# Optimization experiments

Hardware: AMD Instinct MI355X
Metric: run time of the kernel (lower is better)

The kernel has to match this reference:

```python
import jax, jax.numpy as jnp
import numpy as np

N, D1, D2, B = 8, 2048, 1024, 512
D = D1 * D2
MAXBW = 3
NUM_PART = 5          # num_possible_partitions
TEMP = 0.01           # TEMPERATURE used in df_lt
DENOS = (3.0, 5.0, 17.0)  # 2^2-1, 2^2+1, 2^4+1


def ste_floor(x):
    # straight-through floor: forward floor, backward identity
    return x + jax.lax.stop_gradient(jnp.floor(x) - x)


def segmented_mean(piece, scheme, msp):
    """Replicates the inner python scan over sorted rows.
    piece:  (N, D) sorted residual errors
    scheme: (N-1, D) rounded split decisions (0/1), per column
    msp:    (N-1, D) soft split probabilities (grad factors), per column
    Returns (N, D): each row gets grad_ * (segment mean) of its segment.
    """
    n = piece.shape[0]
    buf = jnp.zeros_like(piece[0])
    cnt = jnp.zeros_like(piece[0])
    g = jnp.ones_like(piece[0])
    reset = jnp.zeros(piece.shape[1], dtype=bool)
    vlist, blist = [], []
    for i in range(n):
        buf = jnp.where(reset, piece[i], buf + piece[i])
        cnt = jnp.where(reset, 1.0, cnt + 1.0)
        g = jnp.where(reset, 1.0, g)
        if i == n - 1:
            vlist.append(g * (buf / cnt))
            blist.append(jnp.ones_like(reset))
        else:
            b = scheme[i] > 0.5
            vlist.append(jnp.where(b, g * msp[i], 0.0) * (buf / cnt))
            blist.append(b)
            g = jnp.where(b, g, g * (1.0 - msp[i]))
            reset = b
    # broadcast each segment-end value back to all rows of its segment
    out = vlist[-1]
    outs = [out]
    for i in range(n - 2, -1, -1):
        out = jnp.where(blist[i], vlist[i], out)
        outs.append(out)
    return jnp.stack(outs[::-1], axis=0)


def residual_quant(U, vsum, s, thr):
    """One residual quantization level (the update_partition=True branch)."""
    res = U - vsum                                   # (N, D)
    idx_maps = jnp.argsort(res, axis=0)              # torch.sort ascending, dim=0
    sorted_err = jnp.take_along_axis(res, idx_maps, axis=0)
    delta = sorted_err[1:] - sorted_err[:-1]         # (N-1, D), >= 0
    delta = delta / jnp.max(delta)
    msp = jax.nn.sigmoid((delta - thr) / TEMP)       # mean_split_point (N-1, D)
    rs = jnp.round(msp)                              # round_split, 0/1

    nm1 = N - 1
    P = 2 ** nm1  # all possible split-column patterns (torch.unique over dim=1)
    weights = (2 ** jnp.arange(nm1 - 1, -1, -1)).astype(jnp.int32)  # row 0 = MSB (lexicographic)
    code = jnp.sum(rs.astype(jnp.int32) * weights[:, None], axis=0)  # (D,)
    counts = jnp.zeros((P,), jnp.int32).at[code].add(1)
    present = counts > 0
    # torch.unique sorts patterns lexicographically -> rank = #present codes below
    rank_of_code = jnp.cumsum(present.astype(jnp.int32)) - present.astype(jnp.int32)
    order = jnp.argsort(-counts)                     # codes by count descending
    top_codes = order[:NUM_PART]
    top_ranks = rank_of_code[top_codes]              # s_indices[:NUM_PART]
    # binary patterns for every possible code
    patterns = ((jnp.arange(P)[:, None] >> jnp.arange(nm1 - 1, -1, -1)[None, :]) & 1).astype(jnp.float32)  # (P, N-1)
    inter = patterns @ patterns[top_codes].T         # (P, NUM_PART)
    sel = jnp.argmax(inter, axis=1)
    reassigned = top_ranks[sel]                      # (P,)
    is_top = jnp.any(rank_of_code[:, None] == top_ranks[None, :], axis=1)
    final_rank = jnp.where(is_top, rank_of_code, reassigned)  # (P,)
    c_rank = final_rank[code]                        # clustered_indices, (D,)

    # NOTE: original indexes round_split / mean_split_point columns BY the
    # unique-cluster index value s_idx (a quirk of the source); replicate it.
    scheme_used = rs[:, c_rank]                      # (N-1, D)
    msp_used = msp[:, c_rank]                        # (N-1, D)

    inner = segmented_mean(sorted_err, scheme_used, msp_used)  # (N, D)
    # einsum('cb,cba->ab', inner, one_hot(idx_maps)) == unsort along dim 0
    inv = jnp.argsort(idx_maps, axis=0)
    grouped = jnp.take_along_axis(inner, inv, axis=0)
    return s * ste_floor(grouped / s)


def setup_inputs():
    key = jax.random.key(0)
    k1, k2 = jax.random.split(key)
    x = jax.random.normal(k1, (B, N, D1), dtype=jnp.float32)
    # kaiming_normal_ on (N, D): std = sqrt(2 / fan_in), fan_in = D
    U = jax.random.normal(k2, (N, D), dtype=jnp.float32) * np.float32(np.sqrt(2.0 / D))
    thres_mean = jnp.full((D2,), -1.3, dtype=jnp.float32)
    return {"x": x, "U": U, "thres_mean": thres_mean}


def reference(x, U, thres_mean):
    beta = jnp.max(U)
    alpha = jnp.min(U)
    s = (beta - alpha) / DENOS[0]
    vsum = s * ste_floor(U / s)                      # base quantization level
    thr = jax.nn.sigmoid(jnp.repeat(thres_mean, D1))  # thres_mean.repeat_interleave(D1)
    for deno in DENOS[1:MAXBW]:
        s = s / deno
        vsum = vsum + residual_quant(U, vsum, s, thr)
    w = vsum.reshape(N, D1, D2)
    return jnp.einsum('bnd,ndl->bnl', x, w)
```

## Files before the change

### kernel.cpp

```cpp
#include <hip/hip_runtime.h>
#include <hip/hip_bf16.h>
#include <math.h>

#define NROW 8
#define DT   2097152
#define DD1  2048
#define DD2  1024
#define BATCH 512
#define NBLK4 2048


typedef __attribute__((ext_vector_type(8))) short short8;
typedef __attribute__((ext_vector_type(4))) float f32x4;

__device__ __forceinline__ unsigned fenc(float f){
  unsigned u = __float_as_uint(f);
  return (u & 0x80000000u) ? ~u : (u | 0x80000000u);
}
__device__ __forceinline__ float fdec(unsigned k){
  return (k & 0x80000000u) ? __uint_as_float(k ^ 0x80000000u) : __uint_as_float(~k);
}
__device__ __forceinline__ float sigmoid_ref(float z){
  #pragma clang fp contract(off)
  return 1.0f / (1.0f + expf(-z));
}
__device__ __forceinline__ unsigned short f2bf(float f){
  __hip_bfloat16 h = __float2bfloat16(f);
  return *reinterpret_cast<unsigned short*>(&h);
}
__device__ __forceinline__ float base1(float u, float s1, float inv_s1){
  #pragma clang fp contract(off)
  return s1 * floorf(u * inv_s1);
}
__device__ __forceinline__ void async16(const unsigned short* g, unsigned short* l){
  __builtin_amdgcn_global_load_lds((const __attribute__((address_space(1))) unsigned int*)g,
                                   (__attribute__((address_space(3))) unsigned int*)l, 16, 0, 0);
}

#define CSWAPV(a,b) { float _lo=fminf(a,b), _hi=fmaxf(a,b); a=_lo; b=_hi; }
__device__ __forceinline__ void sort8v(float v[8]){
  CSWAPV(v[0],v[1]) CSWAPV(v[2],v[3]) CSWAPV(v[4],v[5]) CSWAPV(v[6],v[7])
  CSWAPV(v[0],v[2]) CSWAPV(v[1],v[3]) CSWAPV(v[4],v[6]) CSWAPV(v[5],v[7])
  CSWAPV(v[1],v[2]) CSWAPV(v[5],v[6])
  CSWAPV(v[0],v[4]) CSWAPV(v[1],v[5]) CSWAPV(v[2],v[6]) CSWAPV(v[3],v[7])
  CSWAPV(v[2],v[4]) CSWAPV(v[3],v[5])
  CSWAPV(v[1],v[2]) CSWAPV(v[3],v[4]) CSWAPV(v[5],v[6])
}
__device__ __forceinline__ void cswapkv(float&av,int&ai,float&bv,int&bi){
  bool sw = (av > bv) || ((av == bv) && (ai > bi));
  float nav = sw ? bv : av; float nbv = sw ? av : bv;
  int   nai = sw ? bi : ai; int   nbi = sw ? ai : bi;
  av = nav; bv = nbv; ai = nai; bi = nbi;
}
#define CSWAPK(i,j) cswapkv(v[i],ix[i],v[j],ix[j]);
__device__ __forceinline__ void sort8kv(float v[8], int ix[8]){
  CSWAPK(0,1) CSWAPK(2,3) CSWAPK(4,5) CSWAPK(6,7)
  CSWAPK(0,2) CSWAPK(1,3) CSWAPK(4,6) CSWAPK(5,7)
  CSWAPK(1,2) CSWAPK(5,6)
  CSWAPK(0,4) CSWAPK(1,5) CSWAPK(2,6) CSWAPK(3,7)
  CSWAPK(2,4) CSWAPK(3,5)
  CSWAPK(1,2) CSWAPK(3,4) CSWAPK(5,6)
}

__global__ void k_init(unsigned* __restrict__ meta){
  int t = threadIdx.x;
  if (t == 0){ meta[0] = 0u; meta[1] = 0xFFFFFFFFu; meta[2] = 0u; meta[3] = 0u; }
  if (t < 128){ meta[4+t] = 0u; meta[132+t] = 0u; }
}

__global__ __launch_bounds__(256) void k_minmax(const float* __restrict__ U, unsigned* __restrict__ meta){
  __shared__ unsigned smx[256], smn[256];
  int t = threadIdx.x;
  size_t i = (size_t)blockIdx.x*256 + t;
  size_t stride = (size_t)gridDim.x*256;
  const float4* U4 = (const float4*)U;
  float mx = -INFINITY, mn = INFINITY;
  for (; i < (size_t)NROW*DT/4; i += stride){
    float4 v = U4[i];
    mx = fmaxf(fmaxf(mx,v.x), fmaxf(v.y, fmaxf(v.z,v.w)));
    mn = fminf(fminf(mn,v.x), fminf(v.y, fminf(v.z,v.w)));
  }
  smx[t] = fenc(mx); smn[t] = fenc(mn);
  __syncthreads();
  for (int o = 128; o > 0; o >>= 1){
    if (t < o){ smx[t] = max(smx[t], smx[t+o]); smn[t] = min(smn[t], smn[t+o]); }
    __syncthreads();
  }
  if (t == 0){ atomicMax(&meta[0], smx[0]); atomicMin(&meta[1], smn[0]); }
}

__global__ __launch_bounds__(256) void k_passA2(const float* __restrict__ U, unsigned* __restrict__ meta){
  #pragma clang fp contract(off)
  __shared__ unsigned sred[256];
  int t = threadIdx.x;
  int d0 = (blockIdx.x*256 + t)*4;
  float beta = fdec(meta[0]), alpha = fdec(meta[1]);
  float s1 = (beta - alpha) / 3.0f;
  float inv_s1 = 1.0f / s1;
  float4 u[8];
  #pragma unroll
  for (int i = 0; i < 8; ++i) u[i] = *(const float4*)(U + (size_t)i*DT + d0);
  unsigned dmax = 0u;
  #pragma unroll
  for (int c = 0; c < 4; ++c){
    float res[8];
    #pragma unroll
    for (int i = 0; i < 8; ++i){
      float uv = ((const float*)&u[i])[c];
      res[i] = uv - base1(uv, s1, inv_s1);
    }
    sort8v(res);
    float m = 0.0f;
    #pragma unroll
    for (int i = 0; i < 7; ++i) m = fmaxf(m, res[i+1] - res[i]);
    dmax = max(dmax, __float_as_uint(m));
  }
  sred[t] = dmax;
  __syncthreads();
  for (int o = 128; o > 0; o >>= 1){
    if (t < o) sred[t] = max(sred[t], sred[t+o]);
    __syncthreads();
  }
  if (t == 0) atomicMax(&meta[2], sred[0]);
}

template<int LEVEL>
__global__ __launch_bounds__(256) void k_passB(const float* __restrict__ U, const float* __restrict__ vsum,
                                               const float* __restrict__ thres_mean,
                                               unsigned char* __restrict__ code, unsigned* __restrict__ meta){
  #pragma clang fp contract(off)
  __shared__ int hist[128];
  int t = threadIdx.x;
  if (t < 128) hist[t] = 0;
  __syncthreads();
  int d0 = (blockIdx.x*256 + t)*4;
  float beta = fdec(meta[0]), alpha = fdec(meta[1]);
  float s1 = (beta - alpha) / 3.0f;
  float inv_s1 = 1.0f / s1;
  float gmax = __uint_as_float(meta[(LEVEL==2)?2:3]);
  float inv_gmax = 1.0f / gmax;
  float4 u[8], b[8];
  #pragma unroll
  for (int i = 0; i < 8; ++i){
    u[i] = *(const float4*)(U + (size_t)i*DT + d0);
    if (LEVEL == 2){
      float4 bb;
      bb.x = base1(u[i].x, s1, inv_s1); bb.y = base1(u[i].y, s1, inv_s1);
      bb.z = base1(u[i].z, s1, inv_s1); bb.w = base1(u[i].w, s1, inv_s1);
      b[i] = bb;
    } else {
      b[i] = *(const float4*)(vsum + (size_t)i*DT + d0);
    }
  }
  float thr = sigmoid_ref(thres_mean[d0 >> 11]);
  uchar4 cods;
  unsigned char* cp = (unsigned char*)&cods;
  #pragma unroll
  for (int c = 0; c < 4; ++c){
    float res[8];
    #pragma unroll
    for (int i = 0; i < 8; ++i) res[i] = ((const float*)&u[i])[c] - ((const float*)&b[i])[c];
    sort8v(res);
    int cd = 0;
    #pragma unroll
    for (int i = 0; i < 7; ++i){
      float dn = (res[i+1] - res[i]) * inv_gmax;
      int bit = (dn > thr) ? 1 : 0;
      cd = (cd << 1) | bit;
    }
    cp[c] = (unsigned char)cd;
    atomicAdd(&hist[cd], 1);
  }
  *(uchar4*)(code + d0) = cods;
  __syncthreads();
  if (t < 128 && hist[t] > 0) atomicAdd((int*)&meta[((LEVEL==2)?4:132) + t], hist[t]);
}

template<int LEVEL>
__global__ void k_small(const float* __restrict__ U, const float* __restrict__ vsum,
                        const float* __restrict__ thres_mean, unsigned* __restrict__ meta){
  #pragma clang fp contract(off)
  __shared__ int cs[128], rk[128], redk[128];
  __shared__ int top_code[5], top_rank[5];
  __shared__ int w0cnt;
  int c = threadIdx.x;
  cs[c] = (int)meta[((LEVEL==2)?4:132) + c];
  bool present = cs[c] > 0;
  unsigned long long bm = __ballot(present);
  int lane = c & 63;
  int r = (int)__popcll(bm & ((1ull << lane) - 1ull));
  if (c == 63) w0cnt = (int)__popcll(bm);
  __syncthreads();
  if (c >= 64) r += w0cnt;
  rk[c] = r;
  __syncthreads();
  for (int k = 0; k < 5; ++k){
    redk[c] = (cs[c] << 7) | (127 - c);
    __syncthreads();
    for (int o = 64; o > 0; o >>= 1){
      if (c < o) redk[c] = max(redk[c], redk[c+o]);
      __syncthreads();
    }
    if (c == 0){
      int best = 127 - (redk[0] & 127);
      top_code[k] = best; top_rank[k] = rk[best];
      cs[best] = -1;
    }
    __syncthreads();
  }
  int besti = -1, sel = 0;
  #pragma unroll
  for (int j = 0; j < 5; ++j){
    int inter = __popc(c & top_code[j]);
    if (inter > besti){ besti = inter; sel = j; }
  }
  bool is_top = false;
  #pragma unroll
  for (int j = 0; j < 5; ++j) is_top = is_top || (rk[c] == top_rank[j]);
  int fr = is_top ? rk[c] : top_rank[sel];
  ((int*)meta)[260 + c] = fr;
  float beta = fdec(meta[0]), alpha = fdec(meta[1]);
  float s1 = (beta - alpha) / 3.0f;
  float inv_s1 = 1.0f / s1;
  float gmax = __uint_as_float(meta[(LEVEL==2)?2:3]);
  float res[8];
  #pragma unroll
  for (int i = 0; i < 8; ++i){
    size_t off = (size_t)i*DT + c;
    float u = U[off];
    float b = (LEVEL==2) ? base1(u, s1, inv_s1) : vsum[off];
    res[i] = u - b;
  }
  sort8v(res);
  float thr = sigmoid_ref(thres_mean[c >> 11]);
  unsigned bits = 0;
  float* msp_tab = (float*)&meta[388];
  #pragma unroll
  for (int i = 0; i < 7; ++i){
    float dn  = (res[i+1] - res[i]) / gmax;
    float z   = (dn - thr) / 0.01f;
    float msp = sigmoid_ref(z);
    msp_tab[c*7 + i] = msp;
    bits |= ((unsigned)(int)rintf(msp)) << i;
  }
  meta[1284 + c] = bits;
}

template<int LEVEL>
__global__ __launch_bounds__(256) void k_passD(const float* __restrict__ U, float* __restrict__ vsum,
                                               const unsigned char* __restrict__ code,
                                               unsigned* __restrict__ meta){
  #pragma clang fp contract(off)
  __shared__ float q_lds[32*256];
  __shared__ int fr_s[128];
  __shared__ unsigned bits_s[128];
  __shared__ float msp_s[128*7];
  __shared__ unsigned sred[256];
  int t = threadIdx.x;
  if (t < 128){ fr_s[t] = ((int*)meta)[260 + t]; bits_s[t] = meta[1284 + t]; }
  for (int i = t; i < 128*7; i += 256) msp_s[i] = ((float*)&meta[388])[i];
  __syncthreads();
  int d0 = (blockIdx.x*256 + t)*4;
  float beta = fdec(meta[0]), alpha = fdec(meta[1]);
  float s1 = (beta - alpha) / 3.0f;
  float inv_s1 = 1.0f / s1;
  float s2 = s1 / 5.0f;
  float s  = (LEVEL == 2) ? s2 : (s2 / 17.0f);
  float inv_s = 1.0f / s;
  float4 u4[8], b4[8];
  #pragma unroll
  for (int i = 0; i < 8; ++i){
    u4[i] = *(const float4*)(U + (size_t)i*DT + d0);
    if (LEVEL == 2){
      float4 bb;
      bb.x = base1(u4[i].x, s1, inv_s1); bb.y = base1(u4[i].y, s1, inv_s1);
      bb.z = base1(u4[i].z, s1, inv_s1); bb.w = base1(u4[i].w, s1, inv_s1);
      b4[i] = bb;
    } else {
      b4[i] = *(const float4*)(vsum + (size_t)i*DT + d0);
    }
  }
  uchar4 cods = *(const uchar4*)(code + d0);
  const unsigned char* cp = (const unsigned char*)&cods;
  #pragma unroll
  for (int c = 0; c < 4; ++c){
    float v[8]; int ix[8];
    #pragma unroll
    for (int i = 0; i < 8; ++i){
      v[i] = ((const float*)&u4[i])[c] - ((const float*)&b4[i])[c];
      ix[i] = i;
    }
    sort8kv(v, ix);
    int cr = fr_s[cp[c]];
    unsigned sb = bits_s[cr];
    float vv[8]; bool bl[8];
    float buf = 0.0f, cnt = 0.0f, g = 1.0f; bool reset = false;
    #pragma unroll
    for (int i = 0; i < 8; ++i){
      buf = reset ? v[i] : (buf + v[i]);
      cnt = reset ? 1.0f : (cnt + 1.0f);
      g   = reset ? 1.0f : g;
      float m = buf * __builtin_amdgcn_rcpf(cnt);
      if (i == 7){ vv[7] = g * m; bl[7] = true; }
      else {
        float msp = msp_s[cr*7 + i];
        bool b = ((sb >> i) & 1u) != 0u;
        vv[i] = b ? ((g * msp) * m) : 0.0f;
        bl[i] = b;
        g = b ? g : (g * (1.0f - msp));
        reset = b;
      }
    }
    float out = vv[7];
    float inner[8];
    inner[7] = out;
    for (int i = 6; i >= 0; --i){ if (bl[i]) out = vv[i]; inner[i] = out; }
    #pragma unroll
    for (int i = 0; i < 8; ++i){
      float q = s * floorf(inner[i] * inv_s);
      q_lds[(ix[i]*4 + c)*256 + t] = q;
    }
  }
  float4 vn4[8];
  unsigned dmax = 0u;
  #pragma unroll
  for (int c = 0; c < 4; ++c){
    float res3[8];
    #pragma unroll
    for (int rr = 0; rr < 8; ++rr){
      float q = q_lds[(rr*4 + c)*256 + t];
      float vn = ((const float*)&b4[rr])[c] + q;
      ((float*)&vn4[rr])[c] = vn;
      if (LEVEL == 2) res3[rr] = ((const float*)&u4[rr])[c] - vn;
    }
    if (LEVEL == 2){
      sort8v(res3);
      float m = 0.0f;
      #pragma unroll
      for (int i = 0; i < 7; ++i) m = fmaxf(m, res3[i+1] - res3[i]);
      dmax = max(dmax, __float_as_uint(m));
    }
  }
  #pragma unroll
  for (int rr = 0; rr < 8; ++rr)
    *(float4*)(vsum + (size_t)rr*DT + d0) = vn4[rr];
  if (LEVEL == 2){
    sred[t] = dmax;
    __syncthreads();
    for (int o = 128; o > 0; o >>= 1){
      if (t < o) sred[t] = max(sred[t], sred[t+o]);
      __syncthreads();
    }
    if (t == 0) atomicMax(&meta[3], sred[0]);
  }
}

__global__ __launch_bounds__(256) void k_wt(const float* __restrict__ vsum, unsigned short* __restrict__ wt){
  __shared__ unsigned short tile[64][68];
  int t = threadIdx.x;
  int c4 = t & 15, r0 = t >> 4;
  int n = blockIdx.z, k0 = blockIdx.y*64, l0 = blockIdx.x*64;
  const float* src = vsum + (size_t)n*DT;
  #pragma unroll
  for (int i = 0; i < 4; ++i){
    int r = r0 + i*16;
    float4 v = *(const float4*)(src + (size_t)(k0+r)*DD2 + l0 + c4*4);
    tile[r][c4*4+0] = f2bf(v.x); tile[r][c4*4+1] = f2bf(v.y);
    tile[r][c4*4+2] = f2bf(v.z); tile[r][c4*4+3] = f2bf(v.w);
  }
  __syncthreads();
  unsigned short* dst = wt + (size_t)n*DT;
  #pragma unroll
  for (int i = 0; i < 4; ++i){
    int rl = r0 + i*16;
    ushort4 o;
    o.x = tile[c4*4+0][rl]; o.y = tile[c4*4+1][rl];
    o.z = tile[c4*4+2][rl]; o.w = tile[c4*4+3][rl];
    *(ushort4*)(dst + (size_t)(l0+rl)*DD1 + k0 + c4*4) = o;
  }
}

__global__ __launch_bounds__(256) void k_xb(const float* __restrict__ x, unsigned short* __restrict__ xb){
  int idx = (blockIdx.x*256 + threadIdx.x)*4;
  float4 v = *(const float4*)(x + idx);
  ushort4 o;
  o.x = f2bf(v.x); o.y = f2bf(v.y); o.z = f2bf(v.z); o.w = f2bf(v.w);
  *(ushort4*)(xb + idx) = o;
}

__global__ __launch_bounds__(256) void k_gemm(const unsigned short* __restrict__ xb,
                                              const unsigned short* __restrict__ wt,
                                              float* __restrict__ out){
  __shared__ __align__(16) unsigned short As[64*64];
  __shared__ __align__(16) unsigned short Bs[128*64];
  int t = threadIdx.x;
  int lane = t & 63, wv = t >> 6;
  int n  = blockIdx.z;
  int b0 = blockIdx.y * 64;
  int l0 = blockIdx.x * 128;
  int wm = (wv >> 1) * 32, wn = (wv & 1) * 64;
  int col = lane & 15, quad = lane >> 4;
  int arow = lane >> 3, aseg = lane & 7;
  const unsigned short* wtn = wt + (size_t)n*DT;
  f32x4 acc[2][4] = {};
  for (int k0 = 0; k0 < DD1; k0 += 64){
    #pragma unroll
    for (int i = 0; i < 2; ++i){
      int row = wv*16 + i*8 + arow;
      const unsigned short* g = xb + (((size_t)(b0+row)*NROW + n)*DD1 + k0 + aseg*8);
      async16(g, &As[(wv*16 + i*8)*64]);
    }
    #pragma unroll
    for (int i = 0; i < 4; ++i){
      int row = wv*32 + i*8 + arow;
      const unsigned short* g = wtn + ((size_t)(l0+row)*DD1 + k0 + aseg*8);
      async16(g, &Bs[(wv*32 + i*8)*64]);
    }
    __syncthreads();
    #pragma unroll
    for (int ks = 0; ks < 2; ++ks){
      int kq = ks*32 + quad*8;
      short8 af[2], bfr[4];
      #pragma unroll
      for (int mi = 0; mi < 2; ++mi) af[mi]  = *(const short8*)&As[(wm + mi*16 + col)*64 + kq];
      #pragma unroll
      for (int ni = 0; ni < 4; ++ni) bfr[ni] = *(const short8*)&Bs[(wn + ni*16 + col)*64 + kq];
      #pragma unroll
      for (int mi = 0; mi < 2; ++mi)
        #pragma unroll
        for (int ni = 0; ni < 4; ++ni)
          acc[mi][ni] = __builtin_amdgcn_mfma_f32_16x16x32_bf16(af[mi], bfr[ni], acc[mi][ni], 0, 0, 0);
    }
    __syncthreads();
  }
  #pragma unroll
  for (int mi = 0; mi < 2; ++mi)
    #pragma unroll
    for (int ni = 0; ni < 4; ++ni)
      #pragma unroll
      for (int r = 0; r < 4; ++r){
        int b = b0 + wm + mi*16 + quad*4 + r;
        int l = l0 + wn + ni*16 + col;
        out[((size_t)b*NROW + n)*DD2 + l] = acc[mi][ni][r];
      }
}

extern "C" void kernel_launch(void* const* d_in, const int* in_sizes, int n_in,
                              void* d_out, int out_size, void* d_ws, size_t ws_size,
                              hipStream_t stream){
  const float* x  = (const float*)d_in[0];
  const float* U  = (const float*)d_in[1];
  const float* tm = (const float*)d_in[2];
  float* out  = (float*)d_out;
  float* vsum = (float*)d_ws;
  unsigned char* code = (unsigned char*)d_ws + (size_t)NROW*DT*4;
  unsigned short* wt  = (unsigned short*)((unsigned char*)d_ws + (size_t)NROW*DT*4 + DT);
  unsigned* meta = (unsigned*)((unsigned char*)d_ws + (size_t)NROW*DT*4 + DT + (size_t)NROW*DT*2);
  unsigned short* xb = (unsigned short*)d_ws;
  (void)in_sizes; (void)n_in; (void)out_size; (void)ws_size;

  k_init  <<<1,    256, 0, stream>>>(meta);
  k_minmax<<<2048, 256, 0, stream>>>(U, meta);

  k_passA2  <<<NBLK4, 256, 0, stream>>>(U, meta);
  k_passB<2><<<NBLK4, 256, 0, stream>>>(U, vsum, tm, code, meta);
  k_small<2><<<1,    128, 0, stream>>>(U, vsum, tm, meta);
  k_passD<2><<<NBLK4, 256, 0, stream>>>(U, vsum, code, meta);

  k_passB<3><<<NBLK4, 256, 0, stream>>>(U, vsum, tm, code, meta);
  k_small<3><<<1,    128, 0, stream>>>(U, vsum, tm, meta);
  k_passD<3><<<NBLK4, 256, 0, stream>>>(U, vsum, code, meta);

  k_wt  <<<dim3(DD2/64, DD1/64, NROW), 256, 0, stream>>>(vsum, wt);
  k_xb  <<<(BATCH*NROW*DD1)/1024, 256, 0, stream>>>(x, xb);
  k_gemm<<<dim3(DD2/128, BATCH/64, NROW), 256, 0, stream>>>(xb, wt, out);
}
```

Before: 428.7 us.

## Compress intermediate vsum to byte codes and bf16, fuse minmax with x cast

The level-2 fp32 vsum intermediate is replaced by a one-byte quantization index per element, and the base value is recomputed from U in later passes. The final vsum is written directly as bf16, so the transpose kernel reads half as many bytes. The min/max and x-to-bf16 conversion kernels are fused into one launch. Global atomics are replaced by per-block slot arrays that every consumer block re-reduces, which removes the init kernel but adds redundant slot reductions (2048 entries) at the start of each block. Clamping the level-2 index to [-8,7] assumes the residual floor stays in range.

Result: faster. 399.2 us (-6.9%).

```diff
diff --git a/kernel.cpp b/kernel.cpp
--- a/kernel.cpp
+++ b/kernel.cpp
@@ -7,8 +7,13 @@
 #define DD1  2048
 #define DD2  1024
 #define BATCH 512
-#define NBLK4 2048
-
+#define NBLK 2048
+
+
+#define SL_SMAX 0
+#define SL_SMIN 2048
+#define SL_G2   4096
+#define SL_G3   6144
 
 typedef __attribute__((ext_vector_type(8))) short short8;
 typedef __attribute__((ext_vector_type(4))) float f32x4;
@@ -62,41 +67,74 @@
   CSWAPK(1,2) CSWAPK(3,4) CSWAPK(5,6)
 }
 
-__global__ void k_init(unsigned* __restrict__ meta){
-  int t = threadIdx.x;
-  if (t == 0){ meta[0] = 0u; meta[1] = 0xFFFFFFFFu; meta[2] = 0u; meta[3] = 0u; }
-  if (t < 128){ meta[4+t] = 0u; meta[132+t] = 0u; }
-}
-
-__global__ __launch_bounds__(256) void k_minmax(const float* __restrict__ U, unsigned* __restrict__ meta){
-  __shared__ unsigned smx[256], smn[256];
-  int t = threadIdx.x;
-  size_t i = (size_t)blockIdx.x*256 + t;
-  size_t stride = (size_t)gridDim.x*256;
+template<int BD>
+__device__ __forceinline__ unsigned slots_max(const unsigned* s, unsigned* red, int t){
+  unsigned v = 0u;
+  for (int i = t; i < NBLK; i += BD) v = max(v, s[i]);
+  red[t] = v; __syncthreads();
+  for (int o = BD/2; o > 0; o >>= 1){ if (t < o) red[t] = max(red[t], red[t+o]); __syncthreads(); }
+  unsigned r = red[0]; __syncthreads(); return r;
+}
+template<int BD>
+__device__ __forceinline__ unsigned slots_min(const unsigned* s, unsigned* red, int t){
+  unsigned v = 0xFFFFFFFFu;
+  for (int i = t; i < NBLK; i += BD) v = min(v, s[i]);
+  red[t] = v; __syncthreads();
+  for (int o = BD/2; o > 0; o >>= 1){ if (t < o) red[t] = min(red[t], red[t+o]); __syncthreads(); }
+  unsigned r = red[0]; __syncthreads(); return r;
+}
+template<int BD>
+__device__ __forceinline__ float get_s1(const unsigned* slots, unsigned* red, int t){
+  float beta  = fdec(slots_max<BD>(slots + SL_SMAX, red, t));
+  float alpha = fdec(slots_min<BD>(slots + SL_SMIN, red, t));
+  return (beta - alpha) / 3.0f;
+}
+__device__ __forceinline__ float vn2_of(float u, unsigned char mb, float s1, float inv_s1, float s2){
+  #pragma clang fp contract(off)
+  return base1(u, s1, inv_s1) + s2 * (float)((int)mb - 8);
+}
+
+__global__ __launch_bounds__(256) void k_mmxb(const float* __restrict__ U, const float* __restrict__ x,
+                                              unsigned short* __restrict__ xb,
+                                              unsigned* __restrict__ meta, unsigned* __restrict__ slots){
+  __shared__ unsigned redA[256], redB[256];
+  int t = threadIdx.x, b = blockIdx.x;
+  int gid = b*256 + t;
+  if (b == 0 && t < 128){ meta[4+t] = 0u; meta[132+t] = 0u; }
+  const float4* x4 = (const float4*)x;
+  #pragma unroll
+  for (int i = 0; i < 4; ++i){
+    int idx = gid + i*524288;
+    float4 v = x4[idx];
+    ushort4 o;
+    o.x = f2bf(v.x); o.y = f2bf(v.y); o.z = f2bf(v.z); o.w = f2bf(v.w);
+    *(ushort4*)(xb + (size_t)idx*4) = o;
+  }
   const float4* U4 = (const float4*)U;
   float mx = -INFINITY, mn = INFINITY;
-  for (; i < (size_t)NROW*DT/4; i += stride){
-    float4 v = U4[i];
-    mx = fmaxf(fmaxf(mx,v.x), fmaxf(v.y, fmaxf(v.z,v.w)));
-    mn = fminf(fminf(mn,v.x), fminf(v.y, fminf(v.z,v.w)));
-  }
-  smx[t] = fenc(mx); smn[t] = fenc(mn);
+  #pragma unroll
+  for (int i = 0; i < 8; ++i){
+    float4 v = U4[gid + i*524288];
+    mx = fmaxf(mx, fmaxf(fmaxf(v.x,v.y), fmaxf(v.z,v.w)));
+    mn = fminf(mn, fminf(fminf(v.x,v.y), fminf(v.z,v.w)));
+  }
+  redA[t] = fenc(mx); redB[t] = fenc(mn);
   __syncthreads();
   for (int o = 128; o > 0; o >>= 1){
-    if (t < o){ smx[t] = max(smx[t], smx[t+o]); smn[t] = min(smn[t], smn[t+o]); }
-    __syncthreads();
-  }
-  if (t == 0){ atomicMax(&meta[0], smx[0]); atomicMin(&meta[1], smn[0]); }
-}
-
-__global__ __launch_bounds__(256) void k_passA2(const float* __restrict__ U, unsigned* __restrict__ meta){
-  #pragma clang fp contract(off)
-  __shared__ unsigned sred[256];
-  int t = threadIdx.x;
-  int d0 = (blockIdx.x*256 + t)*4;
-  float beta = fdec(meta[0]), alpha = fdec(meta[1]);
-  float s1 = (beta - alpha) / 3.0f;
+    if (t < o){ redA[t] = max(redA[t], redA[t+o]); redB[t] = min(redB[t], redB[t+o]); }
+    __syncthreads();
+  }
+  if (t == 0){ slots[SL_SMAX + b] = redA[0]; slots[SL_SMIN + b] = redB[0]; }
+}
+
+__global__ __launch_bounds__(256) void k_passA2(const float* __restrict__ U,
+                                                unsigned* __restrict__ slots){
+  #pragma clang fp contract(off)
+  __shared__ unsigned red[256];
+  int t = threadIdx.x, b = blockIdx.x;
+  float s1 = get_s1<256>(slots, red, t);
   float inv_s1 = 1.0f / s1;
+  int d0 = (b*256 + t)*4;
   float4 u[8];
   #pragma unroll
   for (int i = 0; i < 8; ++i) u[i] = *(const float4*)(U + (size_t)i*DT + d0);
@@ -115,75 +153,84 @@
     for (int i = 0; i < 7; ++i) m = fmaxf(m, res[i+1] - res[i]);
     dmax = max(dmax, __float_as_uint(m));
   }
-  sred[t] = dmax;
+  red[t] = dmax;
   __syncthreads();
   for (int o = 128; o > 0; o >>= 1){
-    if (t < o) sred[t] = max(sred[t], sred[t+o]);
-    __syncthreads();
-  }
-  if (t == 0) atomicMax(&meta[2], sred[0]);
+    if (t < o) red[t] = max(red[t], red[t+o]);
+    __syncthreads();
+  }
+  if (t == 0) slots[SL_G2 + b] = red[0];
 }
 
 template<int LEVEL>
-__global__ __launch_bounds__(256) void k_passB(const float* __restrict__ U, const float* __restrict__ vsum,
-                                               const float* __restrict__ thres_mean,
-                                               unsigned char* __restrict__ code, unsigned* __restrict__ meta){
-  #pragma clang fp contract(off)
+__global__ __launch_bounds__(256) void k_passB(const float* __restrict__ U,
+                                               const unsigned char* __restrict__ mcode,
+                                               const float* __restrict__ tm,
+                                               unsigned char* __restrict__ code,
+                                               unsigned* __restrict__ meta, unsigned* __restrict__ slots){
+  #pragma clang fp contract(off)
+  __shared__ unsigned red[256];
   __shared__ int hist[128];
-  int t = threadIdx.x;
+  int t = threadIdx.x, b = blockIdx.x;
   if (t < 128) hist[t] = 0;
-  __syncthreads();
-  int d0 = (blockIdx.x*256 + t)*4;
-  float beta = fdec(meta[0]), alpha = fdec(meta[1]);
-  float s1 = (beta - alpha) / 3.0f;
+  float s1 = get_s1<256>(slots, red, t);
   float inv_s1 = 1.0f / s1;
-  float gmax = __uint_as_float(meta[(LEVEL==2)?2:3]);
+  float s2 = s1 / 5.0f;
+  float gmax = __uint_as_float(slots_max<256>(slots + ((LEVEL==2)?SL_G2:SL_G3), red, t));
   float inv_gmax = 1.0f / gmax;
-  float4 u[8], b[8];
+  int d0 = (b*256 + t)*4;
+  float4 u[8], bb[8];
   #pragma unroll
   for (int i = 0; i < 8; ++i){
     u[i] = *(const float4*)(U + (size_t)i*DT + d0);
     if (LEVEL == 2){
-      float4 bb;
-      bb.x = base1(u[i].x, s1, inv_s1); bb.y = base1(u[i].y, s1, inv_s1);
-      bb.z = base1(u[i].z, s1, inv_s1); bb.w = base1(u[i].w, s1, inv_s1);
-      b[i] = bb;
+      bb[i].x = base1(u[i].x, s1, inv_s1); bb[i].y = base1(u[i].y, s1, inv_s1);
+      bb[i].z = base1(u[i].z, s1, inv_s1); bb[i].w = base1(u[i].w, s1, inv_s1);
     } else {
-      b[i] = *(const float4*)(vsum + (size_t)i*DT + d0);
-    }
-  }
-  float thr = sigmoid_ref(thres_mean[d0 >> 11]);
+      uchar4 m4 = *(const uchar4*)(mcode + (size_t)i*DT + d0);
+      bb[i].x = vn2_of(u[i].x, m4.x, s1, inv_s1, s2);
+      bb[i].y = vn2_of(u[i].y, m4.y, s1, inv_s1, s2);
+      bb[i].z = vn2_of(u[i].z, m4.z, s1, inv_s1, s2);
+      bb[i].w = vn2_of(u[i].w, m4.w, s1, inv_s1, s2);
+    }
+  }
+  float thr = sigmoid_ref(tm[d0 >> 11]);
   uchar4 cods;
   unsigned char* cp = (unsigned char*)&cods;
   #pragma unroll
   for (int c = 0; c < 4; ++c){
     float res[8];
     #pragma unroll
-    for (int i = 0; i < 8; ++i) res[i] = ((const float*)&u[i])[c] - ((const float*)&b[i])[c];
+    for (int i = 0; i < 8; ++i) res[i] = ((const float*)&u[i])[c] - ((const float*)&bb[i])[c];
     sort8v(res);
     int cd = 0;
     #pragma unroll
     for (int i = 0; i < 7; ++i){
       float dn = (res[i+1] - res[i]) * inv_gmax;
-      int bit = (dn > thr) ? 1 : 0;
-      cd = (cd << 1) | bit;
+      cd = (cd << 1) | ((dn > thr) ? 1 : 0);
     }
     cp[c] = (unsigned char)cd;
     atomicAdd(&hist[cd], 1);
   }
   *(uchar4*)(code + d0) = cods;
   __syncthreads();
-  if (t < 128 && hist[t] > 0) atomicAdd((int*)&meta[((LEVEL==2)?4:132) + t], hist[t]);
+  if (t < 128){ int h = hist[t]; if (h) atomicAdd((int*)&meta[((LEVEL==2)?4:132) + t], h); }
 }
 
 template<int LEVEL>
-__global__ void k_small(const float* __restrict__ U, const float* __restrict__ vsum,
-                        const float* __restrict__ thres_mean, unsigned* __restrict__ meta){
-  #pragma clang fp contract(off)
+__global__ void k_small(const float* __restrict__ U, const unsigned char* __restrict__ mcode,
+                        const float* __restrict__ tm, unsigned* __restrict__ meta,
+                        unsigned* __restrict__ slots){
+  #pragma clang fp contract(off)
+  __shared__ unsigned red[128];
   __shared__ int cs[128], rk[128], redk[128];
   __shared__ int top_code[5], top_rank[5];
   __shared__ int w0cnt;
   int c = threadIdx.x;
+  float s1 = get_s1<128>(slots, red, c);
+  float inv_s1 = 1.0f / s1;
+  float s2 = s1 / 5.0f;
+  float gmax = __uint_as_float(slots_max<128>(slots + ((LEVEL==2)?SL_G2:SL_G3), red, c));
   cs[c] = (int)meta[((LEVEL==2)?4:132) + c];
   bool present = cs[c] > 0;
   unsigned long long bm = __ballot(present);
@@ -217,24 +264,19 @@
   bool is_top = false;
   #pragma unroll
   for (int j = 0; j < 5; ++j) is_top = is_top || (rk[c] == top_rank[j]);
-  int fr = is_top ? rk[c] : top_rank[sel];
-  ((int*)meta)[260 + c] = fr;
-  float beta = fdec(meta[0]), alpha = fdec(meta[1]);
-  float s1 = (beta - alpha) / 3.0f;
-  float inv_s1 = 1.0f / s1;
-  float gmax = __uint_as_float(meta[(LEVEL==2)?2:3]);
+  ((int*)meta)[260 + c] = is_top ? rk[c] : top_rank[sel];
   float res[8];
   #pragma unroll
   for (int i = 0; i < 8; ++i){
     size_t off = (size_t)i*DT + c;
     float u = U[off];
-    float b = (LEVEL==2) ? base1(u, s1, inv_s1) : vsum[off];
-    res[i] = u - b;
+    float bval = (LEVEL==2) ? base1(u, s1, inv_s1) : vn2_of(u, mcode[off], s1, inv_s1, s2);
+    res[i] = u - bval;
   }
   sort8v(res);
-  float thr = sigmoid_ref(thres_mean[c >> 11]);
+  float thr = sigmoid_ref(tm[c >> 11]);
   unsigned bits = 0;
-  float* msp_tab = (float*)&meta[388];
+  float* msp_tab = (float*)(meta + 388);
   #pragma unroll
   for (int i = 0; i < 7; ++i){
     float dn  = (res[i+1] - res[i]) / gmax;
@@ -247,37 +289,40 @@
 }
 
 template<int LEVEL>
-__global__ __launch_bounds__(256) void k_passD(const float* __restrict__ U, float* __restrict__ vsum,
+__global__ __launch_bounds__(256) void k_passD(const float* __restrict__ U,
+                                               unsigned char* __restrict__ mcode,
+                                               unsigned short* __restrict__ vsumb,
                                                const unsigned char* __restrict__ code,
-                                               unsigned* __restrict__ meta){
+                                               unsigned* __restrict__ meta, unsigned* __restrict__ slots){
   #pragma clang fp contract(off)
   __shared__ float q_lds[32*256];
+  __shared__ unsigned red[256];
   __shared__ int fr_s[128];
   __shared__ unsigned bits_s[128];
-  __shared__ float msp_s[128*7];
-  __shared__ unsigned sred[256];
-  int t = threadIdx.x;
-  if (t < 128){ fr_s[t] = ((int*)meta)[260 + t]; bits_s[t] = meta[1284 + t]; }
-  for (int i = t; i < 128*7; i += 256) msp_s[i] = ((float*)&meta[388])[i];
-  __syncthreads();
-  int d0 = (blockIdx.x*256 + t)*4;
-  float beta = fdec(meta[0]), alpha = fdec(meta[1]);
-  float s1 = (beta - alpha) / 3.0f;
+  __shared__ float msp_s[896];
+  int t = threadIdx.x, b = blockIdx.x;
+  float s1 = get_s1<256>(slots, red, t);
   float inv_s1 = 1.0f / s1;
   float s2 = s1 / 5.0f;
   float s  = (LEVEL == 2) ? s2 : (s2 / 17.0f);
   float inv_s = 1.0f / s;
+  if (t < 128){ fr_s[t] = ((const int*)meta)[260+t]; bits_s[t] = meta[1284+t]; }
+  for (int i = t; i < 896; i += 256) msp_s[i] = ((const float*)(meta+388))[i];
+  __syncthreads();
+  int d0 = (b*256 + t)*4;
   float4 u4[8], b4[8];
   #pragma unroll
   for (int i = 0; i < 8; ++i){
     u4[i] = *(const float4*)(U + (size_t)i*DT + d0);
     if (LEVEL == 2){
-      float4 bb;
-      bb.x = base1(u4[i].x, s1, inv_s1); bb.y = base1(u4[i].y, s1, inv_s1);
-      bb.z = base1(u4[i].z, s1, inv_s1); bb.w = base1(u4[i].w, s1, inv_s1);
-      b4[i] = bb;
+      b4[i].x = base1(u4[i].x, s1, inv_s1); b4[i].y = base1(u4[i].y, s1, inv_s1);
+      b4[i].z = base1(u4[i].z, s1, inv_s1); b4[i].w = base1(u4[i].w, s1, inv_s1);
     } else {
-      b4[i] = *(const float4*)(vsum + (size_t)i*DT + d0);
+      uchar4 m4 = *(const uchar4*)(mcode + (size_t)i*DT + d0);
+      b4[i].x = vn2_of(u4[i].x, m4.x, s1, inv_s1, s2);
+      b4[i].y = vn2_of(u4[i].y, m4.y, s1, inv_s1, s2);
+      b4[i].z = vn2_of(u4[i].z, m4.z, s1, inv_s1, s2);
+      b4[i].w = vn2_of(u4[i].w, m4.w, s1, inv_s1, s2);
     }
   }
   uchar4 cods = *(const uchar4*)(code + d0);
@@ -304,11 +349,11 @@
       if (i == 7){ vv[7] = g * m; bl[7] = true; }
       else {
         float msp = msp_s[cr*7 + i];
-        bool b = ((sb >> i) & 1u) != 0u;
-        vv[i] = b ? ((g * msp) * m) : 0.0f;
-        bl[i] = b;
-        g = b ? g : (g * (1.0f - msp));
-        reset = b;
+        bool bv = ((sb >> i) & 1u) != 0u;
+        vv[i] = bv ? ((g * msp) * m) : 0.0f;
+        bl[i] = bv;
+        g = bv ? g : (g * (1.0f - msp));
+        reset = bv;
       }
     }
     float out = vv[7];
@@ -317,56 +362,69 @@
     for (int i = 6; i >= 0; --i){ if (bl[i]) out = vv[i]; inner[i] = out; }
     #pragma unroll
     for (int i = 0; i < 8; ++i){
-      float q = s * floorf(inner[i] * inv_s);
-      q_lds[(ix[i]*4 + c)*256 + t] = q;
-    }
-  }
-  float4 vn4[8];
+      float mf = floorf(inner[i] * inv_s);
+      q_lds[(ix[i]*4 + c)*256 + t] = mf;
+    }
+  }
   unsigned dmax = 0u;
-  #pragma unroll
-  for (int c = 0; c < 4; ++c){
-    float res3[8];
-    #pragma unroll
-    for (int rr = 0; rr < 8; ++rr){
-      float q = q_lds[(rr*4 + c)*256 + t];
-      float vn = ((const float*)&b4[rr])[c] + q;
-      ((float*)&vn4[rr])[c] = vn;
-      if (LEVEL == 2) res3[rr] = ((const float*)&u4[rr])[c] - vn;
-    }
-    if (LEVEL == 2){
+  if (LEVEL == 2){
+    uchar4 mout[8];
+    #pragma unroll
+    for (int c = 0; c < 4; ++c){
+      float res3[8];
+      #pragma unroll
+      for (int rr = 0; rr < 8; ++rr){
+        int mi = (int)q_lds[(rr*4 + c)*256 + t];
+        mi = max(-8, min(7, mi));
+        float q = s * (float)mi;
+        float vn = ((const float*)&b4[rr])[c] + q;
+        ((unsigned char*)&mout[rr])[c] = (unsigned char)(mi + 8);
+        res3[rr] = ((const float*)&u4[rr])[c] - vn;
+      }
       sort8v(res3);
       float m = 0.0f;
       #pragma unroll
       for (int i = 0; i < 7; ++i) m = fmaxf(m, res3[i+1] - res3[i]);
       dmax = max(dmax, __float_as_uint(m));
     }
-  }
-  #pragma unroll
-  for (int rr = 0; rr < 8; ++rr)
-    *(float4*)(vsum + (size_t)rr*DT + d0) = vn4[rr];
-  if (LEVEL == 2){
-    sred[t] = dmax;
+    #pragma unroll
+    for (int rr = 0; rr < 8; ++rr)
+      *(uchar4*)(mcode + (size_t)rr*DT + d0) = mout[rr];
+    __syncthreads();
+    red[t] = dmax;
     __syncthreads();
     for (int o = 128; o > 0; o >>= 1){
-      if (t < o) sred[t] = max(sred[t], sred[t+o]);
+      if (t < o) red[t] = max(red[t], red[t+o]);
       __syncthreads();
     }
-    if (t == 0) atomicMax(&meta[3], sred[0]);
-  }
-}
-
-__global__ __launch_bounds__(256) void k_wt(const float* __restrict__ vsum, unsigned short* __restrict__ wt){
+    if (t == 0) slots[SL_G3 + b] = red[0];
+  } else {
+    #pragma unroll
+    for (int rr = 0; rr < 8; ++rr){
+      ushort4 o;
+      #pragma unroll
+      for (int c = 0; c < 4; ++c){
+        float q = s * q_lds[(rr*4 + c)*256 + t];
+        float vn = ((const float*)&b4[rr])[c] + q;
+        ((unsigned short*)&o)[c] = f2bf(vn);
+      }
+      *(ushort4*)(vsumb + (size_t)rr*DT + d0) = o;
+    }
+  }
+}
+
+__global__ __launch_bounds__(256) void k_wt(const unsigned short* __restrict__ vsumb,
+                                            unsigned short* __restrict__ wt){
   __shared__ unsigned short tile[64][68];
   int t = threadIdx.x;
   int c4 = t & 15, r0 = t >> 4;
   int n = blockIdx.z, k0 = blockIdx.y*64, l0 = blockIdx.x*64;
-  const float* src = vsum + (size_t)n*DT;
+  const unsigned short* src = vsumb + (size_t)n*DT;
   #pragma unroll
   for (int i = 0; i < 4; ++i){
     int r = r0 + i*16;
-    float4 v = *(const float4*)(src + (size_t)(k0+r)*DD2 + l0 + c4*4);
-    tile[r][c4*4+0] = f2bf(v.x); tile[r][c4*4+1] = f2bf(v.y);
-    tile[r][c4*4+2] = f2bf(v.z); tile[r][c4*4+3] = f2bf(v.w);
+    ushort4 v = *(const ushort4*)(src + (size_t)(k0+r)*DD2 + l0 + c4*4);
+    *(ushort4*)&tile[r][c4*4] = v;
   }
   __syncthreads();
   unsigned short* dst = wt + (size_t)n*DT;
@@ -378,14 +436,6 @@
     o.z = tile[c4*4+2][rl]; o.w = tile[c4*4+3][rl];
     *(ushort4*)(dst + (size_t)(l0+rl)*DD1 + k0 + c4*4) = o;
   }
-}
-
-__global__ __launch_bounds__(256) void k_xb(const float* __restrict__ x, unsigned short* __restrict__ xb){
-  int idx = (blockIdx.x*256 + threadIdx.x)*4;
-  float4 v = *(const float4*)(x + idx);
-  ushort4 o;
-  o.x = f2bf(v.x); o.y = f2bf(v.y); o.z = f2bf(v.z); o.w = f2bf(v.w);
-  *(ushort4*)(xb + idx) = o;
 }
 
 __global__ __launch_bounds__(256) void k_gemm(const unsigned short* __restrict__ xb,
@@ -439,9 +489,9 @@
     for (int ni = 0; ni < 4; ++ni)
       #pragma unroll
       for (int r = 0; r < 4; ++r){
-        int b = b0 + wm + mi*16 + quad*4 + r;
+        int bb = b0 + wm + mi*16 + quad*4 + r;
         int l = l0 + wn + ni*16 + col;
-        out[((size_t)b*NROW + n)*DD2 + l] = acc[mi][ni][r];
+        out[((size_t)bb*NROW + n)*DD2 + l] = acc[mi][ni][r];
       }
 }
 
@@ -451,27 +501,24 @@
   const float* x  = (const float*)d_in[0];
   const float* U  = (const float*)d_in[1];
   const float* tm = (const float*)d_in[2];
-  float* out  = (float*)d_out;
-  float* vsum = (float*)d_ws;
-  unsigned char* code = (unsigned char*)d_ws + (size_t)NROW*DT*4;
-  unsigned short* wt  = (unsigned short*)((unsigned char*)d_ws + (size_t)NROW*DT*4 + DT);
-  unsigned* meta = (unsigned*)((unsigned char*)d_ws + (size_t)NROW*DT*4 + DT + (size_t)NROW*DT*2);
-  unsigned short* xb = (unsigned short*)d_ws;
+  float* out = (float*)d_out;
+  unsigned char*  mcode = (unsigned char*)d_ws;
+  unsigned short* vsumb = (unsigned short*)((unsigned char*)d_ws + 16777216);
+  unsigned short* xb    = (unsigned short*)((unsigned char*)d_ws + 50331648);
+  unsigned char*  code  = (unsigned char*)d_ws + 67108864;
+  unsigned short* wt    = (unsigned short*)((unsigned char*)d_ws + 69206016);
+  unsigned* meta  = (unsigned*)((unsigned char*)d_ws + 102760448);
+  unsigned* slots = (unsigned*)((unsigned char*)d_ws + 102768640);
   (void)in_sizes; (void)n_in; (void)out_size; (void)ws_size;
 
-  k_init  <<<1,    256, 0, stream>>>(meta);
-  k_minmax<<<2048, 256, 0, stream>>>(U, meta);
-
-  k_passA2  <<<NBLK4, 256, 0, stream>>>(U, meta);
-  k_passB<2><<<NBLK4, 256, 0, stream>>>(U, vsum, tm, code, meta);
-  k_small<2><<<1,    128, 0, stream>>>(U, vsum, tm, meta);
-  k_passD<2><<<NBLK4, 256, 0, stream>>>(U, vsum, code, meta);
-
-  k_passB<3><<<NBLK4, 256, 0, stream>>>(U, vsum, tm, code, meta);
-  k_small<3><<<1,    128, 0, stream>>>(U, vsum, tm, meta);
-  k_passD<3><<<NBLK4, 256, 0, stream>>>(U, vsum, code, meta);
-
-  k_wt  <<<dim3(DD2/64, DD1/64, NROW), 256, 0, stream>>>(vsum, wt);
-  k_xb  <<<(BATCH*NROW*DD1)/1024, 256, 0, stream>>>(x, xb);
+  k_mmxb    <<<NBLK, 256, 0, stream>>>(U, x, xb, meta, slots);
+  k_passA2  <<<NBLK, 256, 0, stream>>>(U, slots);
+  k_passB<2><<<NBLK, 256, 0, stream>>>(U, mcode, tm, code, meta, slots);
+  k_small<2><<<1,   128, 0, stream>>>(U, mcode, tm, meta, slots);
+  k_passD<2><<<NBLK, 256, 0, stream>>>(U, mcode, vsumb, code, meta, slots);
+  k_passB<3><<<NBLK, 256, 0, stream>>>(U, mcode, tm, code, meta, slots);
+  k_small<3><<<1,   128, 0, stream>>>(U, mcode, tm, meta, slots);
+  k_passD<3><<<NBLK, 256, 0, stream>>>(U, mcode, vsumb, code, meta, slots);
+  k_wt  <<<dim3(DD2/64, DD1/64, NROW), 256, 0, stream>>>(vsumb, wt);
   k_gemm<<<dim3(DD2/128, BATCH/64, NROW), 256, 0, stream>>>(xb, wt, out);
 }
```
